# Optimization experiments

Measured on AMD Instinct MI355X. Metric: run time of the kernel, lower is better.

The kernel has to match this reference:

```python
import jax, jax.numpy as jnp
import numpy as np

N_HEADS = 8

def setup_inputs() -> dict:
    key = jax.random.key(0)
    qkv = jax.random.normal(key, (4, 1536, 2048), dtype=jnp.float32)
    return {"qkv": qkv}

def reference(qkv):
    bs, width, length = qkv.shape
    ch = width // (3 * N_HEADS)
    q, k, v = jnp.split(qkv, 3, axis=1)  # each [bs, H*C, T]
    scale = 1.0 / np.sqrt(ch).astype(np.float32)
    q = (q * scale).reshape(bs * N_HEADS, ch, length)
    k = k.reshape(bs * N_HEADS, ch, length)
    v = v.reshape(bs * N_HEADS, ch, length)
    weight = jnp.einsum('bct,bcs->bts', q, k)  # [bs*H, T, T]
    weight = jax.nn.softmax(weight.astype(jnp.float32), axis=-1).astype(weight.dtype)
    a = jnp.einsum('bts,bcs->bct', weight, v)  # [bs*H, C, T]
    return a.reshape(bs, -1, length)
```

## Files before the change

kernel.cpp:

```cpp
#include <hip/hip_runtime.h>
#include <hip/hip_bf16.h>

typedef unsigned short u16;
typedef unsigned int uint;
typedef __bf16 bf16x8 __attribute__((ext_vector_type(8)));
typedef float f32x16 __attribute__((ext_vector_type(16)));

#define SEQ 2048
#define DH  64

__device__ __forceinline__ u16 f2bf(float x) {
  __bf16 h = (__bf16)x;
  return __builtin_bit_cast(u16, h);
}

#define FSW(r) ((((r) & 3) << 1) | (((r) >> 2) & 1))

__global__ __launch_bounds__(256) void transpose_qk(const float* __restrict__ qkv,
                                                    u16* __restrict__ qT,
                                                    u16* __restrict__ kT) {
  int idx = blockIdx.x;
  int which = idx >> 10;
  int bh = (idx >> 5) & 31;
  int t0 = (idx & 31) * 64;
  int b = bh >> 3, h = bh & 7;
  const float* src = qkv + ((size_t)(b*1536 + which*512 + h*64)) * SEQ;
  u16* dst = (which ? kT : qT) + (size_t)bh * SEQ * DH;
  float scale = which ? 1.0f : 0.1803368801111244f;

  __shared__ float tile[64][65];
  int tl = threadIdx.x & 63;
  int cw = threadIdx.x >> 6;
#pragma unroll
  for (int i = 0; i < 16; ++i) {
    int c = cw + 4*i;
    tile[c][tl] = src[(size_t)c*SEQ + t0 + tl] * scale;
  }
  __syncthreads();
  int cl2 = (threadIdx.x & 31) * 2;
  int tw  = threadIdx.x >> 5;
#pragma unroll
  for (int i = 0; i < 8; ++i) {
    int t = tw + 8*i;
    unsigned int lo = f2bf(tile[cl2][t]);
    unsigned int hi = f2bf(tile[cl2+1][t]);
    *(unsigned int*)(dst + (size_t)(t0 + t)*DH + cl2) = lo | (hi << 16);
  }
}

__global__ __launch_bounds__(256) void convert_v(const float* __restrict__ qkv,
                                                 u16* __restrict__ v) {
  int row = blockIdx.x;
  int bh = row >> 6, c = row & 63;
  int b = bh >> 3, h = bh & 7;
  const float4* src = (const float4*)(qkv + ((size_t)(b*1536 + 1024 + h*64 + c)) * SEQ);
  u16* dst = v + (size_t)row * SEQ;
  int tid = threadIdx.x;
  float4 a = src[tid*2];
  float4 bq = src[tid*2+1];
  union { u16 u[8]; int4 v4; } pk;
  pk.u[0]=f2bf(a.x); pk.u[1]=f2bf(a.y); pk.u[2]=f2bf(a.z); pk.u[3]=f2bf(a.w);
  pk.u[4]=f2bf(bq.x); pk.u[5]=f2bf(bq.y); pk.u[6]=f2bf(bq.z); pk.u[7]=f2bf(bq.w);
  *(int4*)(dst + tid*8) = pk.v4;
}

__global__ __launch_bounds__(256, 4) void attn(const u16* __restrict__ qT,
                                               const u16* __restrict__ kT,
                                               const u16* __restrict__ vB,
                                               float* __restrict__ out) {
  const int lb = (blockIdx.x & 7) * 128 + (blockIdx.x >> 3);
  const int bh = lb >> 5;
  const int t0 = (lb & 31) * 64;
  const int tid  = threadIdx.x;
  const int wave = tid >> 6;
  const int th   = wave & 1;
  const int sh   = wave >> 1;
  const int lane = tid & 63;
  const int l31  = lane & 31;
  const int hi   = lane >> 5;

  __shared__ __align__(16) u16 smem[2][2][64*64];

  const u16* qrow = qT + ((size_t)bh*SEQ + (t0 + th*32 + l31)) * DH;
  bf16x8 bq[4];
#pragma unroll
  for (int kb = 0; kb < 4; ++kb) bq[kb] = *(const bf16x8*)(qrow + kb*16 + hi*8);

  const u16* ksrc0 = kT + (size_t)bh*SEQ*DH;
  const u16* vsrc0 = vB + (size_t)bh*DH*SEQ;
  const int ci0 = (wave*2+0)*64 + lane;
  const int ci1 = (wave*2+1)*64 + lane;
  const int kr0 = ci0 >> 3, kc0 = ci0 & 7;
  const int kr1 = ci1 >> 3, kc1 = ci1 & 7;
  const u16* kg0 = ksrc0 + (size_t)kr0*DH + ((kc0 ^ FSW(kr0)) * 8);
  const u16* kg1 = ksrc0 + (size_t)kr1*DH + ((kc1 ^ FSW(kr1)) * 8);
  const u16* vg0 = vsrc0 + (size_t)kr0*SEQ + ((kc0 ^ FSW(kr0)) * 8);
  const u16* vg1 = vsrc0 + (size_t)kr1*SEQ + ((kc1 ^ FSW(kr1)) * 8);

#define GLDS(src, dst) __builtin_amdgcn_global_load_lds(                        \
    (const __attribute__((address_space(1))) unsigned int*)(src),               \
    (__attribute__((address_space(3))) unsigned int*)(dst), 16, 0, 0)
#define STAGE(b, sbase) do {                                                    \
    GLDS(kg0 + (size_t)(sbase)*DH, &smem[b][0][ci0*8]);                         \
    GLDS(kg1 + (size_t)(sbase)*DH, &smem[b][0][ci1*8]);                         \
    GLDS(vg0 + (sbase),            &smem[b][1][ci0*8]);                         \
    GLDS(vg1 + (sbase),            &smem[b][1][ci1*8]);                         \
  } while (0)

  f32x16 acc0 = {}, acc1 = {};
  float l_run = 0.f;
  const int fl = FSW(l31);

  STAGE(0, 0);
  __syncthreads();

  int buf = 0;
  for (int s0 = 0; s0 < SEQ; s0 += 64) {
    if (s0 + 64 < SEQ) STAGE(buf ^ 1, s0 + 64);

    const u16* kb_ = &smem[buf][0][0];
    const u16* vb_ = &smem[buf][1][0];

    f32x16 S0 = {};
    __builtin_amdgcn_s_setprio(1);
#pragma unroll
    for (int kb = 0; kb < 4; ++kb) {
      bf16x8 a = *(const bf16x8*)(kb_ + (sh*32 + l31)*64 + (((2*kb+hi) ^ fl) * 8));
      S0 = __builtin_amdgcn_mfma_f32_32x32x16_bf16(a, bq[kb], S0, 0, 0, 0);
    }
    __builtin_amdgcn_s_setprio(0);

    float p0[16];
#pragma unroll
    for (int i = 0; i < 16; ++i) p0[i] = __builtin_amdgcn_exp2f(S0[i]);
    {
      float sm[8];
#pragma unroll
      for (int i = 0; i < 8; ++i) sm[i] = p0[i] + p0[i+8];
#pragma unroll
      for (int i = 0; i < 4; ++i) sm[i] += sm[i+4];
      float ls = (sm[0] + sm[1]) + (sm[2] + sm[3]);
      ls += __shfl_xor(ls, 32);
      l_run += ls;
    }

    uint d0[8];
#pragma unroll
    for (int q = 0; q < 4; ++q)
#pragma unroll
      for (int e = 0; e < 2; ++e) {
        asm("v_cvt_pk_bf16_f32 %0, %1, %2" : "=v"(d0[2*q+e]) : "v"(p0[4*q+2*e]), "v"(p0[4*q+2*e+1]));
      }
    bf16x8 pf[2];
#pragma unroll
    for (int kb2 = 0; kb2 < 2; ++kb2) {
      uint X0 = d0[4*kb2+0], X1 = d0[4*kb2+1];
      uint Y0 = d0[4*kb2+2], Y1 = d0[4*kb2+3];
      asm("v_permlane32_swap_b32 %0, %1" : "+v"(X0), "+v"(Y0));
      asm("v_permlane32_swap_b32 %0, %1" : "+v"(X1), "+v"(Y1));
      uint4 u = {X0, X1, Y0, Y1};
      pf[kb2] = __builtin_bit_cast(bf16x8, u);
    }

    __builtin_amdgcn_s_setprio(1);
#pragma unroll
    for (int ks2 = 0; ks2 < 2; ++ks2) {
      bf16x8 av0 = *(const bf16x8*)(vb_ + l31*64      + (((sh*4 + ks2*2 + hi) ^ fl) * 8));
      bf16x8 av1 = *(const bf16x8*)(vb_ + (32+l31)*64 + (((sh*4 + ks2*2 + hi) ^ fl) * 8));
      acc0 = __builtin_amdgcn_mfma_f32_32x32x16_bf16(av0, pf[ks2], acc0, 0, 0, 0);
      acc1 = __builtin_amdgcn_mfma_f32_32x32x16_bf16(av1, pf[ks2], acc1, 0, 0, 0);
    }
    __builtin_amdgcn_s_setprio(0);

    __syncthreads();
    buf ^= 1;
  }
#undef STAGE
#undef GLDS

  float* ep = (float*)&smem[0][0][0];
  float* lp = ep + 4*1024;
  if (sh == 1) {
    float* b0 = ep + (th*2+0)*1024 + lane;
    float* b1 = ep + (th*2+1)*1024 + lane;
#pragma unroll
    for (int r = 0; r < 16; ++r) { b0[r*64] = acc0[r]; b1[r*64] = acc1[r]; }
    lp[th*64 + lane] = l_run;
  }
  __syncthreads();
  if (sh == 0) {
    const float* b0 = ep + (th*2+0)*1024 + lane;
    const float* b1 = ep + (th*2+1)*1024 + lane;
#pragma unroll
    for (int r = 0; r < 16; ++r) { acc0[r] += b0[r*64]; acc1[r] += b1[r*64]; }
    float lt = l_run + lp[th*64 + lane];
    float linv = 1.0f / lt;
    float* ob = out + (size_t)(bh*64) * SEQ + t0 + th*32 + l31;
#pragma unroll
    for (int r = 0; r < 16; ++r) {
      int c0 = (r & 3) + 8*(r >> 2) + 4*hi;
      ob[(size_t)c0 * SEQ]        = acc0[r] * linv;
      ob[(size_t)(32 + c0) * SEQ] = acc1[r] * linv;
    }
  }
}

extern "C" void kernel_launch(void* const* d_in, const int* in_sizes, int n_in,
                              void* d_out, int out_size, void* d_ws, size_t ws_size,
                              hipStream_t stream) {
  const float* qkv = (const float*)d_in[0];
  float* out = (float*)d_out;
  u16* qT = (u16*)d_ws;
  u16* kT = qT + (size_t)32*SEQ*DH;
  u16* vB = kT + (size_t)32*SEQ*DH;
  transpose_qk<<<2048, 256, 0, stream>>>(qkv, qT, kT);
  convert_v<<<2048, 256, 0, stream>>>(qkv, vB);
  attn<<<1024, 256, 0, stream>>>(qT, kT, vB, out);
}
```

Measured before the change: 65.56 us.

## Drop LDS staging in attention; load K/V directly from global in MFMA-ready tiled layout

The attention loop no longer stages K and V through double-buffered LDS with global_load_lds and per-iteration barriers. Each wave now reads its MFMA operands straight from global memory. To make those reads contiguous, convert_v writes V in a blocked 64x64 tile layout. This removes LDS traffic, swizzling and __syncthreads, but every wave now fetches K/V from L2/global separately, with no shared reuse and no software prefetch to hide latency.

```diff
diff --git a/kernel.cpp b/kernel.cpp
--- a/kernel.cpp
+++ b/kernel.cpp
@@ -13,8 +13,6 @@
   __bf16 h = (__bf16)x;
   return __builtin_bit_cast(u16, h);
 }
-
-#define FSW(r) ((((r) & 3) << 1) | (((r) >> 2) & 1))
 
 __global__ __launch_bounds__(256) void transpose_qk(const float* __restrict__ qkv,
                                                     u16* __restrict__ qT,
@@ -49,24 +47,24 @@
 }
 
 __global__ __launch_bounds__(256) void convert_v(const float* __restrict__ qkv,
-                                                 u16* __restrict__ v) {
+                                                 u16* __restrict__ vT) {
   int row = blockIdx.x;
   int bh = row >> 6, c = row & 63;
   int b = bh >> 3, h = bh & 7;
   const float4* src = (const float4*)(qkv + ((size_t)(b*1536 + 1024 + h*64 + c)) * SEQ);
-  u16* dst = v + (size_t)row * SEQ;
+  u16* dstb = vT + (size_t)bh*SEQ*DH + c*64;
   int tid = threadIdx.x;
   float4 a = src[tid*2];
   float4 bq = src[tid*2+1];
   union { u16 u[8]; int4 v4; } pk;
   pk.u[0]=f2bf(a.x); pk.u[1]=f2bf(a.y); pk.u[2]=f2bf(a.z); pk.u[3]=f2bf(a.w);
   pk.u[4]=f2bf(bq.x); pk.u[5]=f2bf(bq.y); pk.u[6]=f2bf(bq.z); pk.u[7]=f2bf(bq.w);
-  *(int4*)(dst + tid*8) = pk.v4;
+  *(int4*)(dstb + (tid >> 3)*4096 + (tid & 7)*8) = pk.v4;
 }
 
 __global__ __launch_bounds__(256, 4) void attn(const u16* __restrict__ qT,
                                                const u16* __restrict__ kT,
-                                               const u16* __restrict__ vB,
+                                               const u16* __restrict__ vT,
                                                float* __restrict__ out) {
   const int lb = (blockIdx.x & 7) * 128 + (blockIdx.x >> 3);
   const int bh = lb >> 5;
@@ -79,55 +77,37 @@
   const int l31  = lane & 31;
   const int hi   = lane >> 5;
 
-  __shared__ __align__(16) u16 smem[2][2][64*64];
+  __shared__ float ep[4*1024 + 128];
 
   const u16* qrow = qT + ((size_t)bh*SEQ + (t0 + th*32 + l31)) * DH;
   bf16x8 bq[4];
 #pragma unroll
   for (int kb = 0; kb < 4; ++kb) bq[kb] = *(const bf16x8*)(qrow + kb*16 + hi*8);
 
-  const u16* ksrc0 = kT + (size_t)bh*SEQ*DH;
-  const u16* vsrc0 = vB + (size_t)bh*DH*SEQ;
-  const int ci0 = (wave*2+0)*64 + lane;
-  const int ci1 = (wave*2+1)*64 + lane;
-  const int kr0 = ci0 >> 3, kc0 = ci0 & 7;
-  const int kr1 = ci1 >> 3, kc1 = ci1 & 7;
-  const u16* kg0 = ksrc0 + (size_t)kr0*DH + ((kc0 ^ FSW(kr0)) * 8);
-  const u16* kg1 = ksrc0 + (size_t)kr1*DH + ((kc1 ^ FSW(kr1)) * 8);
-  const u16* vg0 = vsrc0 + (size_t)kr0*SEQ + ((kc0 ^ FSW(kr0)) * 8);
-  const u16* vg1 = vsrc0 + (size_t)kr1*SEQ + ((kc1 ^ FSW(kr1)) * 8);
-
-#define GLDS(src, dst) __builtin_amdgcn_global_load_lds(                        \
-    (const __attribute__((address_space(1))) unsigned int*)(src),               \
-    (__attribute__((address_space(3))) unsigned int*)(dst), 16, 0, 0)
-#define STAGE(b, sbase) do {                                                    \
-    GLDS(kg0 + (size_t)(sbase)*DH, &smem[b][0][ci0*8]);                         \
-    GLDS(kg1 + (size_t)(sbase)*DH, &smem[b][0][ci1*8]);                         \
-    GLDS(vg0 + (sbase),            &smem[b][1][ci0*8]);                         \
-    GLDS(vg1 + (sbase),            &smem[b][1][ci1*8]);                         \
-  } while (0)
+  const u16* kbase = kT + (size_t)bh*SEQ*DH + (sh*32 + l31)*DH + hi*8;
+  const u16* vbase = vT + (size_t)bh*SEQ*DH + l31*64 + sh*32 + hi*8;
 
   f32x16 acc0 = {}, acc1 = {};
   float l_run = 0.f;
-  const int fl = FSW(l31);
 
-  STAGE(0, 0);
-  __syncthreads();
-
-  int buf = 0;
   for (int s0 = 0; s0 < SEQ; s0 += 64) {
-    if (s0 + 64 < SEQ) STAGE(buf ^ 1, s0 + 64);
-
-    const u16* kb_ = &smem[buf][0][0];
-    const u16* vb_ = &smem[buf][1][0];
+    const u16* kp = kbase + (size_t)s0*DH;
+    const u16* vp = vbase + (size_t)(s0 >> 6)*4096;
+    bf16x8 ak0 = *(const bf16x8*)(kp);
+    bf16x8 ak1 = *(const bf16x8*)(kp + 16);
+    bf16x8 ak2 = *(const bf16x8*)(kp + 32);
+    bf16x8 ak3 = *(const bf16x8*)(kp + 48);
+    bf16x8 av00 = *(const bf16x8*)(vp);
+    bf16x8 av01 = *(const bf16x8*)(vp + 16);
+    bf16x8 av10 = *(const bf16x8*)(vp + 2048);
+    bf16x8 av11 = *(const bf16x8*)(vp + 2048 + 16);
 
     f32x16 S0 = {};
     __builtin_amdgcn_s_setprio(1);
-#pragma unroll
-    for (int kb = 0; kb < 4; ++kb) {
-      bf16x8 a = *(const bf16x8*)(kb_ + (sh*32 + l31)*64 + (((2*kb+hi) ^ fl) * 8));
-      S0 = __builtin_amdgcn_mfma_f32_32x32x16_bf16(a, bq[kb], S0, 0, 0, 0);
-    }
+    S0 = __builtin_amdgcn_mfma_f32_32x32x16_bf16(ak0, bq[0], S0, 0, 0, 0);
+    S0 = __builtin_amdgcn_mfma_f32_32x32x16_bf16(ak1, bq[1], S0, 0, 0, 0);
+    S0 = __builtin_amdgcn_mfma_f32_32x32x16_bf16(ak2, bq[2], S0, 0, 0, 0);
+    S0 = __builtin_amdgcn_mfma_f32_32x32x16_bf16(ak3, bq[3], S0, 0, 0, 0);
     __builtin_amdgcn_s_setprio(0);
 
     float p0[16];
@@ -163,22 +143,13 @@
     }
 
     __builtin_amdgcn_s_setprio(1);
-#pragma unroll
-    for (int ks2 = 0; ks2 < 2; ++ks2) {
-      bf16x8 av0 = *(const bf16x8*)(vb_ + l31*64      + (((sh*4 + ks2*2 + hi) ^ fl) * 8));
-      bf16x8 av1 = *(const bf16x8*)(vb_ + (32+l31)*64 + (((sh*4 + ks2*2 + hi) ^ fl) * 8));
-      acc0 = __builtin_amdgcn_mfma_f32_32x32x16_bf16(av0, pf[ks2], acc0, 0, 0, 0);
-      acc1 = __builtin_amdgcn_mfma_f32_32x32x16_bf16(av1, pf[ks2], acc1, 0, 0, 0);
-    }
+    acc0 = __builtin_amdgcn_mfma_f32_32x32x16_bf16(av00, pf[0], acc0, 0, 0, 0);
+    acc0 = __builtin_amdgcn_mfma_f32_32x32x16_bf16(av01, pf[1], acc0, 0, 0, 0);
+    acc1 = __builtin_amdgcn_mfma_f32_32x32x16_bf16(av10, pf[0], acc1, 0, 0, 0);
+    acc1 = __builtin_amdgcn_mfma_f32_32x32x16_bf16(av11, pf[1], acc1, 0, 0, 0);
     __builtin_amdgcn_s_setprio(0);
+  }
 
-    __syncthreads();
-    buf ^= 1;
-  }
-#undef STAGE
-#undef GLDS
-
-  float* ep = (float*)&smem[0][0][0];
   float* lp = ep + 4*1024;
   if (sh == 1) {
     float* b0 = ep + (th*2+0)*1024 + lane;
@@ -212,8 +183,8 @@
   float* out = (float*)d_out;
   u16* qT = (u16*)d_ws;
   u16* kT = qT + (size_t)32*SEQ*DH;
-  u16* vB = kT + (size_t)32*SEQ*DH;
+  u16* vT = kT + (size_t)32*SEQ*DH;
   transpose_qk<<<2048, 256, 0, stream>>>(qkv, qT, kT);
-  convert_v<<<2048, 256, 0, stream>>>(qkv, vB);
-  attn<<<1024, 256, 0, stream>>>(qT, kT, vB, out);
+  convert_v<<<2048, 256, 0, stream>>>(qkv, vT);
+  attn<<<1024, 256, 0, stream>>>(qT, kT, vT, out);
 }
```

Result: slower. 136.1 us (+107.6%).
